# Kernel optimization log

Measured on AMD Instinct MI355X. Metric: run time of the kernel, lower is better.

## Reference

```python
import jax, jax.numpy as jnp
import numpy as np

DIM = 1024
HEADS = 16
DIM_HEAD = 64
INNER = HEADS * DIM_HEAD  # 1024
EPS = 1e-5


def setup_inputs() -> dict:
    key = jax.random.key(0)
    ks = jax.random.split(key, 10)
    b, n1, n2 = 8, 4096, 64
    x = jax.random.normal(ks[0], (b, n1, DIM), dtype=jnp.float32)
    latents = jax.random.normal(ks[1], (b, n2, DIM), dtype=jnp.float32)
    attention_mask = jax.random.randint(ks[2], (b, n1, 1), 0, 2).astype(jnp.float32)
    ln1_g = jnp.ones((DIM,), jnp.float32)
    ln1_b = jnp.zeros((DIM,), jnp.float32)
    ln2_g = jnp.ones((DIM,), jnp.float32)
    ln2_b = jnp.zeros((DIM,), jnp.float32)
    Wq = jax.random.normal(ks[3], (DIM, INNER), dtype=jnp.float32) * 0.02
    Wkv = jax.random.normal(ks[4], (DIM, 2 * INNER), dtype=jnp.float32) * 0.02
    Wout = jax.random.normal(ks[5], (INNER, DIM), dtype=jnp.float32) * 0.02
    return {"x": x, "latents": latents, "attention_mask": attention_mask,
            "ln1_g": ln1_g, "ln1_b": ln1_b, "ln2_g": ln2_g, "ln2_b": ln2_b,
            "Wq": Wq, "Wkv": Wkv, "Wout": Wout}


def _layernorm(t, g, b):
    mu = jnp.mean(t, axis=-1, keepdims=True)
    var = jnp.mean(jnp.square(t - mu), axis=-1, keepdims=True)
    return (t - mu) * jax.lax.rsqrt(var + EPS) * g + b


def _split_heads(t):
    b, n, _ = t.shape
    return t.reshape(b, n, HEADS, DIM_HEAD).transpose(0, 2, 1, 3)  # (b,h,n,d)


def reference(x, latents, attention_mask, ln1_g, ln1_b, ln2_g, ln2_b, Wq, Wkv, Wout):
    xn = _layernorm(x, ln1_g, ln1_b)
    ln = _layernorm(latents, ln2_g, ln2_b)
    b, l, _ = ln.shape

    q = ln @ Wq                                   # (b, n2, inner)
    kv_input = jnp.concatenate([xn, ln], axis=1)  # (b, n1+n2, dim)
    kv = kv_input @ Wkv
    k, v = jnp.split(kv, 2, axis=-1)

    q = _split_heads(q)   # (b,h,n2,d)
    k = _split_heads(k)   # (b,h,n1+n2,d)
    v = _split_heads(v)

    scale = 1.0 / np.sqrt(np.sqrt(DIM_HEAD)).astype(np.float32)
    weight = jnp.einsum('bhqd,bhkd->bhqk', q * scale, k * scale)

    # build additive mask: (b,n1,1) -> (b,1,n1), concat ones for latent keys
    m = jnp.swapaxes(attention_mask, 1, 2)                     # (b,1,n1)
    m = jnp.concatenate([m, jnp.ones_like(m[:, :, :1]).repeat(l, axis=2)], axis=2)
    bias = ((m - 1.0) * 100.0)[:, None]                        # (b,1,1,n1+n2)
    weight = weight + bias

    weight = jax.nn.softmax(weight.astype(jnp.float32), axis=-1).astype(weight.dtype)
    out = jnp.einsum('bhqk,bhkd->bhqd', weight, v)
    out = out.transpose(0, 2, 1, 3).reshape(b, l, INNER)
    return out @ Wout
```

## Files before the change

kernel.cpp:

```cpp
#include <hip/hip_runtime.h>
#include <cstdint>
#include <cstddef>


typedef unsigned short u16;
typedef __bf16 bf16x8 __attribute__((ext_vector_type(8)));
typedef float f32x16 __attribute__((ext_vector_type(16)));

#define MFMA32(a, b, c) __builtin_amdgcn_mfma_f32_32x32x16_bf16((a), (b), (c), 0, 0, 0)

__device__ __forceinline__ u16 f2bf(float f) {
  unsigned u = __builtin_bit_cast(unsigned, f);
  u += 0x7FFFu + ((u >> 16) & 1u);
  return (u16)(u >> 16);
}

__device__ __forceinline__ f32x16 zero16() {
  f32x16 z;
#pragma unroll
  for (int i = 0; i < 16; ++i) z[i] = 0.f;
  return z;
}

#if defined(__has_builtin)
#if __has_builtin(__builtin_amdgcn_global_load_lds)
#define HAVE_GLDS 1
#endif
#endif

__device__ __forceinline__ void async16(const u16* g, u16* lbase, int lane) {
#ifdef HAVE_GLDS
  typedef const __attribute__((address_space(1))) void* gp_t;
  typedef __attribute__((address_space(3))) void* lp_t;
  __builtin_amdgcn_global_load_lds((gp_t)g, (lp_t)lbase, 16, 0, 0);
#else
  *(uint4*)(lbase + lane * 8) = *(const uint4*)g;
#endif
}

__global__ void wtrans(const float* __restrict__ W, u16* __restrict__ Wt, int K, int N) {
  __shared__ float t[32][33];
  int n0 = blockIdx.x * 32, k0 = blockIdx.y * 32;
  int tx = threadIdx.x, ty = threadIdx.y;
#pragma unroll
  for (int i = 0; i < 4; ++i)
    t[ty + 8 * i][tx] = W[(size_t)(k0 + ty + 8 * i) * N + n0 + tx];
  __syncthreads();
#pragma unroll
  for (int i = 0; i < 4; ++i)
    Wt[(size_t)(n0 + ty + 8 * i) * K + k0 + tx] = f2bf(t[tx][ty + 8 * i]);
}

__global__ void ln_kernel(const float* __restrict__ x, const float* __restrict__ lat,
                          const float* __restrict__ g1, const float* __restrict__ b1,
                          const float* __restrict__ g2, const float* __restrict__ b2,
                          u16* __restrict__ kvin, u16* __restrict__ qin) {
  int row = blockIdx.x;
  const float *src, *g, *bb;
  u16 *dst, *dst2 = nullptr;
  if (row < 32768) {
    int b = row >> 12, pos = row & 4095;
    src = x + (size_t)row * 1024;
    dst = kvin + (size_t)(b * 4160 + pos) * 1024;
    g = g1; bb = b1;
  } else {
    int i = row - 32768;
    int b = i >> 6, j = i & 63;
    src = lat + (size_t)i * 1024;
    dst = kvin + (size_t)(b * 4160 + 4096 + j) * 1024;
    dst2 = qin + (size_t)i * 1024;
    g = g2; bb = b2;
  }
  int t = threadIdx.x;
  float4 v = *(const float4*)(src + t * 4);
  float s = v.x + v.y + v.z + v.w;
  float ss = v.x * v.x + v.y * v.y + v.z * v.z + v.w * v.w;
#pragma unroll
  for (int off = 32; off; off >>= 1) {
    s += __shfl_xor(s, off);
    ss += __shfl_xor(ss, off);
  }
  __shared__ float red[8];
  int w = t >> 6;
  if ((t & 63) == 0) { red[w] = s; red[w + 4] = ss; }
  __syncthreads();
  s = red[0] + red[1] + red[2] + red[3];
  ss = red[4] + red[5] + red[6] + red[7];
  float mu = s * (1.f / 1024.f);
  float var = ss * (1.f / 1024.f) - mu * mu;
  float rstd = rsqrtf(var + 1e-5f);
  float4 gv = *(const float4*)(g + t * 4);
  float4 bv = *(const float4*)(bb + t * 4);
  ushort4 o;
  o.x = f2bf((v.x - mu) * rstd * gv.x + bv.x);
  o.y = f2bf((v.y - mu) * rstd * gv.y + bv.y);
  o.z = f2bf((v.z - mu) * rstd * gv.z + bv.z);
  o.w = f2bf((v.w - mu) * rstd * gv.w + bv.w);
  *(ushort4*)(dst + t * 4) = o;
  if (dst2) *(ushort4*)(dst2 + t * 4) = o;
}

template <int EPI>
__global__ void __launch_bounds__(256, 2) gemm128(
    const u16* __restrict__ A, const u16* __restrict__ Bt, int K,
    u16* __restrict__ oK, u16* __restrict__ oV, float* __restrict__ oF) {
  __shared__ __align__(16) u16 lds[18432];
  u16* As = lds;
  u16* Bs = lds + 8192;
  const int tid = threadIdx.x;
  const int lane = tid & 63;
  const int w = tid >> 6;
  const int lc = lane & 31;
  const int hh = lane >> 5;
  const int m0 = blockIdx.y * 128;
  const int n0 = blockIdx.x * 128;
  const int wm = (w >> 1) * 64;
  const int wn = (w & 1) * 64;

  f32x16 acc[2][2];
#pragma unroll
  for (int i = 0; i < 2; ++i)
#pragma unroll
    for (int j = 0; j < 2; ++j) acc[i][j] = zero16();

  const int rsub = lane >> 3;
  const int cslot = lane & 7;

  for (int kt = 0; kt < K; kt += 64) {
    __syncthreads();
#pragma unroll
    for (int i = 0; i < 4; ++i) {
      const int rr = (w * 4 + i) * 8 + rsub;
      const int cA = cslot ^ (rr & 7);
      async16(A + (size_t)(m0 + rr) * K + kt + cA * 8, As + (w * 4 + i) * 512, lane);
      async16(Bt + (size_t)(n0 + rr) * K + kt + cA * 8, Bs + (w * 4 + i) * 512, lane);
    }
    __syncthreads();
    const int am0 = wm + lc, am1 = wm + 32 + lc;
    const int bn0 = wn + lc, bn1 = wn + 32 + lc;
#pragma unroll
    for (int s = 0; s < 4; ++s) {
      const int c = s * 2 + hh;
      bf16x8 a0 = *(const bf16x8*)(As + am0 * 64 + ((c ^ (am0 & 7)) * 8));
      bf16x8 a1 = *(const bf16x8*)(As + am1 * 64 + ((c ^ (am1 & 7)) * 8));
      bf16x8 b0 = *(const bf16x8*)(Bs + bn0 * 64 + ((c ^ (bn0 & 7)) * 8));
      bf16x8 b1 = *(const bf16x8*)(Bs + bn1 * 64 + ((c ^ (bn1 & 7)) * 8));
      acc[0][0] = MFMA32(a0, b0, acc[0][0]);
      acc[0][1] = MFMA32(a0, b1, acc[0][1]);
      acc[1][0] = MFMA32(a1, b0, acc[1][0]);
      acc[1][1] = MFMA32(a1, b1, acc[1][1]);
    }
  }

  if constexpr (EPI == 2) {
#pragma unroll
    for (int mt = 0; mt < 2; ++mt)
#pragma unroll
      for (int nt = 0; nt < 2; ++nt)
#pragma unroll
        for (int r = 0; r < 16; ++r) {
          int grow = m0 + wm + mt * 32 + (r & 3) + 8 * (r >> 2) + 4 * hh;
          int gcol = n0 + wn + nt * 32 + lc;
          oF[(size_t)grow * 1024 + gcol] = acc[mt][nt][r];
        }
  } else {
    const bool kstyle = (EPI == 1) || (blockIdx.x < 8);
    if (kstyle) {
      constexpr int SEQ = (EPI == 1) ? 64 : 4160;
      constexpr float SC = (EPI == 1) ? 0.125f : 1.0f;
#pragma unroll
      for (int mt = 0; mt < 2; ++mt)
#pragma unroll
        for (int nt = 0; nt < 2; ++nt)
#pragma unroll
          for (int r = 0; r < 16; ++r) {
            int grow = m0 + wm + mt * 32 + (r & 3) + 8 * (r >> 2) + 4 * hh;
            int gcol = n0 + wn + nt * 32 + lc;
            int bb = grow / SEQ, rr2 = grow - bb * SEQ;
            int h = gcol >> 6, d = gcol & 63;
            oK[(((size_t)(bb * 16 + h)) * SEQ + rr2) * 64 + d] = f2bf(acc[mt][nt][r] * SC);
          }
    } else {
      __syncthreads();
      u16* T = lds;
#pragma unroll
      for (int mt = 0; mt < 2; ++mt)
#pragma unroll
        for (int nt = 0; nt < 2; ++nt) {
          int nl = wn + nt * 32 + lc;
#pragma unroll
          for (int r4 = 0; r4 < 4; ++r4) {
            int ml = wm + mt * 32 + 8 * r4 + 4 * hh;
            ushort4 pk;
            pk.x = f2bf(acc[mt][nt][4 * r4 + 0]);
            pk.y = f2bf(acc[mt][nt][4 * r4 + 1]);
            pk.z = f2bf(acc[mt][nt][4 * r4 + 2]);
            pk.w = f2bf(acc[mt][nt][4 * r4 + 3]);
            *(ushort4*)(T + nl * 144 + ml) = pk;
          }
        }
      __syncthreads();
#pragma unroll
      for (int rr2 = 0; rr2 < 8; ++rr2) {
        int sig = tid + rr2 * 256;
        int n = sig >> 4, cm = (sig & 15) << 3;
        uint4 v = *(const uint4*)(T + n * 144 + cm);
        int gcol = n0 + n - 1024;
        int h = gcol >> 6, d = gcol & 63;
        int grow = m0 + cm;
        int bb = grow / 4160, key = grow - bb * 4160;
        *(uint4*)(oV + (((size_t)(bb * 16 + h)) * 64 + d) * 4160 + key) = v;
      }
    }
  }
}

__global__ void __launch_bounds__(256) attn_kernel(
    const u16* __restrict__ Q, const u16* __restrict__ Kb,
    const u16* __restrict__ Vt, const float* __restrict__ mask,
    float* __restrict__ nums, float* __restrict__ dens) {
  __shared__ __align__(16) u16 Ps[16384];
  __shared__ float Osum[4160];
  __shared__ float den_s[256];
  const int p = blockIdx.x;
  const int bh = p >> 2, s = p & 3;
  const int b = bh >> 4;
  const int tid = threadIdx.x, lane = tid & 63, w = tid >> 6;
  const int hh = lane >> 5, lc = lane & 31;

  for (int i = tid; i < 4160; i += 256) Osum[i] = 0.f;
  den_s[tid] = 0.f;
  __syncthreads();

  const u16* Qb = Q + (size_t)bh * 4096;
  const u16* Kbb = Kb + (size_t)bh * 266240;
  const u16* Vtb = Vt + (size_t)bh * 266240;

  bf16x8 qf[2][4];
#pragma unroll
  for (int qt = 0; qt < 2; ++qt)
#pragma unroll
    for (int ks = 0; ks < 4; ++ks)
      qf[qt][ks] = *(const bf16x8*)(Qb + (qt * 32 + lc) * 64 + ks * 16 + hh * 8);

  f32x16 o[2][2];
#pragma unroll
  for (int i = 0; i < 2; ++i)
#pragma unroll
    for (int j = 0; j < 2; ++j) o[i][j] = zero16();
  float den0 = 0.f, den1 = 0.f;
  u16* Pw = Ps + w * 4096;
  const int t0 = (s == 0) ? 0 : (16 * s + 1);
  const int t1 = (s == 3) ? 65 : (16 * (s + 1) + 1);

  for (int t = t0 + w; t < t1; t += 4) {
    const int key0 = t * 64;
    const int keyl = key0 + lane;
    float bias_v = 0.f;
    if (keyl < 4096) bias_v = (mask[b * 4096 + keyl] - 1.f) * 100.f;

    bf16x8 kf[2][4];
#pragma unroll
    for (int ktt = 0; ktt < 2; ++ktt)
#pragma unroll
      for (int ks = 0; ks < 4; ++ks)
        kf[ktt][ks] = *(const bf16x8*)(Kbb + (size_t)(key0 + ktt * 32 + lc) * 64 + ks * 16 + hh * 8);

    f32x16 st[2][2];
#pragma unroll
    for (int i = 0; i < 2; ++i)
#pragma unroll
      for (int j = 0; j < 2; ++j) st[i][j] = zero16();
#pragma unroll
    for (int ks = 0; ks < 4; ++ks) {
      st[0][0] = MFMA32(kf[0][ks], qf[0][ks], st[0][0]);
      st[0][1] = MFMA32(kf[0][ks], qf[1][ks], st[0][1]);
      st[1][0] = MFMA32(kf[1][ks], qf[0][ks], st[1][0]);
      st[1][1] = MFMA32(kf[1][ks], qf[1][ks], st[1][1]);
    }

#pragma unroll
    for (int ktt = 0; ktt < 2; ++ktt) {
      float bb[16];
#pragma unroll
      for (int r = 0; r < 16; ++r)
        bb[r] = __shfl(bias_v, ktt * 32 + (r & 3) + 8 * (r >> 2) + 4 * hh);
#pragma unroll
      for (int qt = 0; qt < 2; ++qt) {
        const int q = qt * 32 + lc;
        float dsum = 0.f;
#pragma unroll
        for (int r4 = 0; r4 < 4; ++r4) {
          float e0 = __expf(st[ktt][qt][4 * r4 + 0] + bb[4 * r4 + 0]);
          float e1 = __expf(st[ktt][qt][4 * r4 + 1] + bb[4 * r4 + 1]);
          float e2 = __expf(st[ktt][qt][4 * r4 + 2] + bb[4 * r4 + 2]);
          float e3 = __expf(st[ktt][qt][4 * r4 + 3] + bb[4 * r4 + 3]);
          dsum += e0 + e1 + e2 + e3;
          ushort4 pk;
          pk.x = f2bf(e0); pk.y = f2bf(e1); pk.z = f2bf(e2); pk.w = f2bf(e3);
          const int c = ktt * 4 + r4;
          *(ushort4*)(Pw + q * 64 + ((c ^ (q & 7)) * 8) + 4 * hh) = pk;
        }
        if (qt == 0) den0 += dsum; else den1 += dsum;
      }
    }

#pragma unroll
    for (int ks = 0; ks < 4; ++ks) {
      const int c = ks * 2 + hh;
      bf16x8 p0 = *(const bf16x8*)(Pw + lc * 64 + ((c ^ (lc & 7)) * 8));
      bf16x8 p1 = *(const bf16x8*)(Pw + (32 + lc) * 64 + ((c ^ (lc & 7)) * 8));
      bf16x8 v0 = *(const bf16x8*)(Vtb + (size_t)lc * 4160 + key0 + ks * 16 + hh * 8);
      bf16x8 v1 = *(const bf16x8*)(Vtb + (size_t)(32 + lc) * 4160 + key0 + ks * 16 + hh * 8);
      o[0][0] = MFMA32(p0, v0, o[0][0]);
      o[0][1] = MFMA32(p0, v1, o[0][1]);
      o[1][0] = MFMA32(p1, v0, o[1][0]);
      o[1][1] = MFMA32(p1, v1, o[1][1]);
    }
  }

#pragma unroll
  for (int qt = 0; qt < 2; ++qt)
#pragma unroll
    for (int dt = 0; dt < 2; ++dt)
#pragma unroll
      for (int r = 0; r < 16; ++r) {
        int row = qt * 32 + (r & 3) + 8 * (r >> 2) + 4 * hh;
        int col = dt * 32 + lc;
        atomicAdd(&Osum[row * 65 + col], o[qt][dt][r]);
      }
  den0 += __shfl_xor(den0, 32);
  den1 += __shfl_xor(den1, 32);
  if (lane < 32) {
    den_s[w * 64 + lc] = den0;
    den_s[w * 64 + 32 + lc] = den1;
  }
  __syncthreads();
  float* np_ = nums + (size_t)p * 4096;
  for (int i = tid; i < 4096; i += 256)
    np_[i] = Osum[(i >> 6) * 65 + (i & 63)];
  if (tid < 64)
    dens[p * 64 + tid] = den_s[tid] + den_s[64 + tid] + den_s[128 + tid] + den_s[192 + tid];
}

__global__ void combine_kernel(const float* __restrict__ nums, const float* __restrict__ dens,
                               u16* __restrict__ O) {
  int idx = blockIdx.x * 256 + threadIdx.x;
  int bh = idx >> 12;
  int q = (idx >> 6) & 63, d = idx & 63;
  float n = 0.f, dn = 0.f;
#pragma unroll
  for (int s = 0; s < 4; ++s) {
    n += nums[(size_t)(bh * 4 + s) * 4096 + q * 64 + d];
    dn += dens[(bh * 4 + s) * 64 + q];
  }
  int b = bh >> 4, h = bh & 15;
  O[((size_t)(b * 64 + q) * 16 + h) * 64 + d] = f2bf(n / dn);
}

extern "C" void kernel_launch(void* const* d_in, const int* in_sizes, int n_in,
                              void* d_out, int out_size, void* d_ws, size_t ws_size,
                              hipStream_t stream) {
  (void)in_sizes; (void)n_in; (void)out_size; (void)ws_size;
  const float* x    = (const float*)d_in[0];
  const float* lat  = (const float*)d_in[1];
  const float* mask = (const float*)d_in[2];
  const float* g1   = (const float*)d_in[3];
  const float* b1   = (const float*)d_in[4];
  const float* g2   = (const float*)d_in[5];
  const float* b2   = (const float*)d_in[6];
  const float* Wq   = (const float*)d_in[7];
  const float* Wkv  = (const float*)d_in[8];
  const float* Wout = (const float*)d_in[9];
  float* out = (float*)d_out;

  unsigned char* w = (unsigned char*)d_ws;
  u16* kvin = (u16*)w;   w += (size_t)33280 * 1024 * 2;
  u16* qin = (u16*)w;    w += (size_t)512 * 1024 * 2;
  u16* WqT = (u16*)w;    w += (size_t)1024 * 1024 * 2;
  u16* WkvT = (u16*)w;   w += (size_t)2048 * 1024 * 2;
  u16* WoutT = (u16*)w;  w += (size_t)1024 * 1024 * 2;
  u16* Kbuf = (u16*)w;   w += (size_t)33280 * 1024 * 2;
  u16* Vtb = (u16*)w;    w += (size_t)33280 * 1024 * 2;
  u16* Qbuf = (u16*)w;   w += (size_t)512 * 1024 * 2;
  u16* Obuf = (u16*)w;   w += (size_t)512 * 1024 * 2;
  float* nums = (float*)w; w += (size_t)512 * 4096 * 4;
  float* dens = (float*)w; w += (size_t)512 * 64 * 4;

  wtrans<<<dim3(32, 32), dim3(32, 8), 0, stream>>>(Wq, WqT, 1024, 1024);
  wtrans<<<dim3(64, 32), dim3(32, 8), 0, stream>>>(Wkv, WkvT, 1024, 2048);
  wtrans<<<dim3(32, 32), dim3(32, 8), 0, stream>>>(Wout, WoutT, 1024, 1024);
  ln_kernel<<<33280, 256, 0, stream>>>(x, lat, g1, b1, g2, b2, kvin, qin);
  gemm128<0><<<dim3(16, 260), 256, 0, stream>>>(kvin, WkvT, 1024, Kbuf, Vtb, nullptr);
  gemm128<1><<<dim3(8, 4), 256, 0, stream>>>(qin, WqT, 1024, Qbuf, nullptr, nullptr);
  attn_kernel<<<512, 256, 0, stream>>>(Qbuf, Kbuf, Vtb, mask, nums, dens);
  combine_kernel<<<2048, 256, 0, stream>>>(nums, dens, Obuf);
  gemm128<2><<<dim3(8, 4), 256, 0, stream>>>(Obuf, WoutT, 1024, nullptr, nullptr, out);
}
```

Before: 501.1 us.

## Stage K/V tiles in LDS for attention, split-K small GEMMs, merge weight transposes

The attention kernel now double-buffers 64-key K and V tiles into LDS with async loads, and all four waves share each tile instead of each wave streaming its own keys from global memory. V is written by the KV GEMM in a tiled 64x64 blocked layout to support this. The small Q and output projections become split-K GEMMs with 4 K-slices plus separate reduce kernels, so they launch 128 blocks instead of 32. The three weight transposes are merged into one launch. The cost is extra launches, partial-sum traffic through global memory, and two block barriers per key tile in attention.

```diff
diff --git a/kernel.cpp b/kernel.cpp
--- a/kernel.cpp
+++ b/kernel.cpp
@@ -38,9 +38,18 @@
 #endif
 }
 
-__global__ void wtrans(const float* __restrict__ W, u16* __restrict__ Wt, int K, int N) {
+__global__ void wtrans_all(const float* __restrict__ Wq, const float* __restrict__ Wkv,
+                           const float* __restrict__ Wout, u16* __restrict__ WqT,
+                           u16* __restrict__ WkvT, u16* __restrict__ WoutT) {
   __shared__ float t[32][33];
-  int n0 = blockIdx.x * 32, k0 = blockIdx.y * 32;
+  const int z = blockIdx.z;
+  const float* W;
+  u16* Wt;
+  int N, nbase;
+  if (z == 0) { W = Wq; Wt = WqT; N = 1024; nbase = 0; }
+  else if (z == 3) { W = Wout; Wt = WoutT; N = 1024; nbase = 0; }
+  else { W = Wkv; Wt = WkvT; N = 2048; nbase = (z - 1) * 1024; }
+  int n0 = nbase + blockIdx.x * 32, k0 = blockIdx.y * 32;
   int tx = threadIdx.x, ty = threadIdx.y;
 #pragma unroll
   for (int i = 0; i < 4; ++i)
@@ -48,7 +57,7 @@
   __syncthreads();
 #pragma unroll
   for (int i = 0; i < 4; ++i)
-    Wt[(size_t)(n0 + ty + 8 * i) * K + k0 + tx] = f2bf(t[tx][ty + 8 * i]);
+    Wt[(size_t)(n0 + ty + 8 * i) * 1024 + k0 + tx] = f2bf(t[tx][ty + 8 * i]);
 }
 
 __global__ void ln_kernel(const float* __restrict__ x, const float* __restrict__ lat,
@@ -102,7 +111,7 @@
 
 template <int EPI>
 __global__ void __launch_bounds__(256, 2) gemm128(
-    const u16* __restrict__ A, const u16* __restrict__ Bt, int K,
+    const u16* __restrict__ A, const u16* __restrict__ Bt, int kLen,
     u16* __restrict__ oK, u16* __restrict__ oV, float* __restrict__ oF) {
   __shared__ __align__(16) u16 lds[18432];
   u16* As = lds;
@@ -116,6 +125,7 @@
   const int n0 = blockIdx.x * 128;
   const int wm = (w >> 1) * 64;
   const int wn = (w & 1) * 64;
+  const int k0 = blockIdx.z * kLen;
 
   f32x16 acc[2][2];
 #pragma unroll
@@ -126,14 +136,14 @@
   const int rsub = lane >> 3;
   const int cslot = lane & 7;
 
-  for (int kt = 0; kt < K; kt += 64) {
+  for (int kt = k0; kt < k0 + kLen; kt += 64) {
     __syncthreads();
 #pragma unroll
     for (int i = 0; i < 4; ++i) {
       const int rr = (w * 4 + i) * 8 + rsub;
       const int cA = cslot ^ (rr & 7);
-      async16(A + (size_t)(m0 + rr) * K + kt + cA * 8, As + (w * 4 + i) * 512, lane);
-      async16(Bt + (size_t)(n0 + rr) * K + kt + cA * 8, Bs + (w * 4 + i) * 512, lane);
+      async16(A + (size_t)(m0 + rr) * 1024 + kt + cA * 8, As + (w * 4 + i) * 512, lane);
+      async16(Bt + (size_t)(n0 + rr) * 1024 + kt + cA * 8, Bs + (w * 4 + i) * 512, lane);
     }
     __syncthreads();
     const int am0 = wm + lc, am1 = wm + 32 + lc;
@@ -153,6 +163,7 @@
   }
 
   if constexpr (EPI == 2) {
+    oF += (size_t)blockIdx.z * (512 * 1024);
 #pragma unroll
     for (int mt = 0; mt < 2; ++mt)
 #pragma unroll
@@ -164,10 +175,7 @@
           oF[(size_t)grow * 1024 + gcol] = acc[mt][nt][r];
         }
   } else {
-    const bool kstyle = (EPI == 1) || (blockIdx.x < 8);
-    if (kstyle) {
-      constexpr int SEQ = (EPI == 1) ? 64 : 4160;
-      constexpr float SC = (EPI == 1) ? 0.125f : 1.0f;
+    if (blockIdx.x < 8) {
 #pragma unroll
       for (int mt = 0; mt < 2; ++mt)
 #pragma unroll
@@ -176,9 +184,9 @@
           for (int r = 0; r < 16; ++r) {
             int grow = m0 + wm + mt * 32 + (r & 3) + 8 * (r >> 2) + 4 * hh;
             int gcol = n0 + wn + nt * 32 + lc;
-            int bb = grow / SEQ, rr2 = grow - bb * SEQ;
+            int bb = grow / 4160, rr2 = grow - bb * 4160;
             int h = gcol >> 6, d = gcol & 63;
-            oK[(((size_t)(bb * 16 + h)) * SEQ + rr2) * 64 + d] = f2bf(acc[mt][nt][r] * SC);
+            oK[(((size_t)(bb * 16 + h)) * 4160 + rr2) * 64 + d] = f2bf(acc[mt][nt][r]);
           }
     } else {
       __syncthreads();
@@ -209,138 +217,135 @@
         int h = gcol >> 6, d = gcol & 63;
         int grow = m0 + cm;
         int bb = grow / 4160, key = grow - bb * 4160;
-        *(uint4*)(oV + (((size_t)(bb * 16 + h)) * 64 + d) * 4160 + key) = v;
+        int tt = key >> 6, kk = key & 63;
+        *(uint4*)(oV + ((((size_t)(bb * 16 + h) * 65 + tt) * 64 + d) * 64 + kk)) = v;
       }
     }
   }
+}
+
+__global__ void qreduce(const float* __restrict__ P, u16* __restrict__ Qbuf) {
+  int idx = blockIdx.x * 256 + threadIdx.x;
+  float s = P[idx] + P[idx + 524288] + P[idx + 2 * 524288] + P[idx + 3 * 524288];
+  int row = idx >> 10, col = idx & 1023;
+  int b = row >> 6, q = row & 63, h = col >> 6, d = col & 63;
+  Qbuf[((size_t)(b * 16 + h) * 64 + q) * 64 + d] = f2bf(s * 0.125f);
+}
+
+__global__ void oreduce(const float* __restrict__ P, float* __restrict__ out) {
+  int idx = blockIdx.x * 256 + threadIdx.x;
+  out[idx] = P[idx] + P[idx + 524288] + P[idx + 2 * 524288] + P[idx + 3 * 524288];
 }
 
 __global__ void __launch_bounds__(256) attn_kernel(
     const u16* __restrict__ Q, const u16* __restrict__ Kb,
-    const u16* __restrict__ Vt, const float* __restrict__ mask,
+    const u16* __restrict__ VB, const float* __restrict__ mask,
     float* __restrict__ nums, float* __restrict__ dens) {
-  __shared__ __align__(16) u16 Ps[16384];
-  __shared__ float Osum[4160];
-  __shared__ float den_s[256];
+  __shared__ __align__(16) u16 KT[2][4096];
+  __shared__ __align__(16) u16 VT[2][4096];
+  __shared__ __align__(16) u16 PT[4096];
+  __shared__ float den_s[128];
   const int p = blockIdx.x;
   const int bh = p >> 2, s = p & 3;
   const int b = bh >> 4;
   const int tid = threadIdx.x, lane = tid & 63, w = tid >> 6;
   const int hh = lane >> 5, lc = lane & 31;
-
-  for (int i = tid; i < 4160; i += 256) Osum[i] = 0.f;
-  den_s[tid] = 0.f;
-  __syncthreads();
+  const int rsub = lane >> 3, cslot = lane & 7;
+  const int kh = w >> 1, qh = w & 1;
+  const int qh2 = w >> 1, dh2 = w & 1;
 
   const u16* Qb = Q + (size_t)bh * 4096;
   const u16* Kbb = Kb + (size_t)bh * 266240;
-  const u16* Vtb = Vt + (size_t)bh * 266240;
-
-  bf16x8 qf[2][4];
-#pragma unroll
-  for (int qt = 0; qt < 2; ++qt)
-#pragma unroll
-    for (int ks = 0; ks < 4; ++ks)
-      qf[qt][ks] = *(const bf16x8*)(Qb + (qt * 32 + lc) * 64 + ks * 16 + hh * 8);
-
-  f32x16 o[2][2];
-#pragma unroll
-  for (int i = 0; i < 2; ++i)
-#pragma unroll
-    for (int j = 0; j < 2; ++j) o[i][j] = zero16();
-  float den0 = 0.f, den1 = 0.f;
-  u16* Pw = Ps + w * 4096;
+  const u16* Vbb = VB + (size_t)bh * 266240;
+
+  bf16x8 qf[4];
+#pragma unroll
+  for (int ks = 0; ks < 4; ++ks)
+    qf[ks] = *(const bf16x8*)(Qb + (qh * 32 + lc) * 64 + ks * 16 + hh * 8);
+
+  f32x16 o = zero16();
+  float den_reg = 0.f;
   const int t0 = (s == 0) ? 0 : (16 * s + 1);
-  const int t1 = (s == 3) ? 65 : (16 * (s + 1) + 1);
-
-  for (int t = t0 + w; t < t1; t += 4) {
-    const int key0 = t * 64;
-    const int keyl = key0 + lane;
+  const int t1 = (s == 3) ? 65 : (16 * s + 17);
+
+  auto stage = [&](int t, int buf) {
+    const u16* ksrc = Kbb + (size_t)t * 4096;
+    const u16* vsrc = Vbb + (size_t)t * 4096;
+    const int soff = rsub * 64 + ((cslot ^ rsub) * 8);
+#pragma unroll
+    for (int i = 0; i < 2; ++i) {
+      const int c = w * 2 + i;
+      async16(ksrc + c * 512 + soff, KT[buf] + c * 512, lane);
+      async16(vsrc + c * 512 + soff, VT[buf] + c * 512, lane);
+    }
+  };
+
+  stage(t0, 0);
+  for (int t = t0; t < t1; ++t) {
+    const int buf = (t - t0) & 1;
+    __syncthreads();
+    if (t + 1 < t1) stage(t + 1, buf ^ 1);
+
     float bias_v = 0.f;
-    if (keyl < 4096) bias_v = (mask[b * 4096 + keyl] - 1.f) * 100.f;
-
-    bf16x8 kf[2][4];
-#pragma unroll
-    for (int ktt = 0; ktt < 2; ++ktt)
-#pragma unroll
-      for (int ks = 0; ks < 4; ++ks)
-        kf[ktt][ks] = *(const bf16x8*)(Kbb + (size_t)(key0 + ktt * 32 + lc) * 64 + ks * 16 + hh * 8);
-
-    f32x16 st[2][2];
-#pragma unroll
-    for (int i = 0; i < 2; ++i)
-#pragma unroll
-      for (int j = 0; j < 2; ++j) st[i][j] = zero16();
-#pragma unroll
-    for (int ks = 0; ks < 4; ++ks) {
-      st[0][0] = MFMA32(kf[0][ks], qf[0][ks], st[0][0]);
-      st[0][1] = MFMA32(kf[0][ks], qf[1][ks], st[0][1]);
-      st[1][0] = MFMA32(kf[1][ks], qf[0][ks], st[1][0]);
-      st[1][1] = MFMA32(kf[1][ks], qf[1][ks], st[1][1]);
-    }
-
-#pragma unroll
-    for (int ktt = 0; ktt < 2; ++ktt) {
-      float bb[16];
-#pragma unroll
-      for (int r = 0; r < 16; ++r)
-        bb[r] = __shfl(bias_v, ktt * 32 + (r & 3) + 8 * (r >> 2) + 4 * hh);
-#pragma unroll
-      for (int qt = 0; qt < 2; ++qt) {
-        const int q = qt * 32 + lc;
-        float dsum = 0.f;
-#pragma unroll
-        for (int r4 = 0; r4 < 4; ++r4) {
-          float e0 = __expf(st[ktt][qt][4 * r4 + 0] + bb[4 * r4 + 0]);
-          float e1 = __expf(st[ktt][qt][4 * r4 + 1] + bb[4 * r4 + 1]);
-          float e2 = __expf(st[ktt][qt][4 * r4 + 2] + bb[4 * r4 + 2]);
-          float e3 = __expf(st[ktt][qt][4 * r4 + 3] + bb[4 * r4 + 3]);
-          dsum += e0 + e1 + e2 + e3;
-          ushort4 pk;
-          pk.x = f2bf(e0); pk.y = f2bf(e1); pk.z = f2bf(e2); pk.w = f2bf(e3);
-          const int c = ktt * 4 + r4;
-          *(ushort4*)(Pw + q * 64 + ((c ^ (q & 7)) * 8) + 4 * hh) = pk;
-        }
-        if (qt == 0) den0 += dsum; else den1 += dsum;
-      }
-    }
-
+    {
+      int key_l = t * 64 + kh * 32 + lc;
+      if (key_l < 4096) bias_v = (mask[b * 4096 + key_l] - 1.f) * 100.f;
+    }
+
+    f32x16 st = zero16();
+    const int R = kh * 32 + lc;
 #pragma unroll
     for (int ks = 0; ks < 4; ++ks) {
       const int c = ks * 2 + hh;
-      bf16x8 p0 = *(const bf16x8*)(Pw + lc * 64 + ((c ^ (lc & 7)) * 8));
-      bf16x8 p1 = *(const bf16x8*)(Pw + (32 + lc) * 64 + ((c ^ (lc & 7)) * 8));
-      bf16x8 v0 = *(const bf16x8*)(Vtb + (size_t)lc * 4160 + key0 + ks * 16 + hh * 8);
-      bf16x8 v1 = *(const bf16x8*)(Vtb + (size_t)(32 + lc) * 4160 + key0 + ks * 16 + hh * 8);
-      o[0][0] = MFMA32(p0, v0, o[0][0]);
-      o[0][1] = MFMA32(p0, v1, o[0][1]);
-      o[1][0] = MFMA32(p1, v0, o[1][0]);
-      o[1][1] = MFMA32(p1, v1, o[1][1]);
-    }
-  }
-
-#pragma unroll
-  for (int qt = 0; qt < 2; ++qt)
-#pragma unroll
-    for (int dt = 0; dt < 2; ++dt)
-#pragma unroll
-      for (int r = 0; r < 16; ++r) {
-        int row = qt * 32 + (r & 3) + 8 * (r >> 2) + 4 * hh;
-        int col = dt * 32 + lc;
-        atomicAdd(&Osum[row * 65 + col], o[qt][dt][r]);
-      }
-  den0 += __shfl_xor(den0, 32);
-  den1 += __shfl_xor(den1, 32);
-  if (lane < 32) {
-    den_s[w * 64 + lc] = den0;
-    den_s[w * 64 + 32 + lc] = den1;
-  }
+      bf16x8 kfr = *(const bf16x8*)(KT[buf] + R * 64 + ((c ^ (R & 7)) * 8));
+      st = MFMA32(kfr, qf[ks], st);
+    }
+
+    const int q = qh * 32 + lc;
+    float dsum = 0.f;
+#pragma unroll
+    for (int r4 = 0; r4 < 4; ++r4) {
+      float bb0 = __shfl(bias_v, 0 + 8 * r4 + 4 * hh);
+      float bb1 = __shfl(bias_v, 1 + 8 * r4 + 4 * hh);
+      float bb2 = __shfl(bias_v, 2 + 8 * r4 + 4 * hh);
+      float bb3 = __shfl(bias_v, 3 + 8 * r4 + 4 * hh);
+      float e0 = __expf(st[4 * r4 + 0] + bb0);
+      float e1 = __expf(st[4 * r4 + 1] + bb1);
+      float e2 = __expf(st[4 * r4 + 2] + bb2);
+      float e3 = __expf(st[4 * r4 + 3] + bb3);
+      dsum += e0 + e1 + e2 + e3;
+      ushort4 pk;
+      pk.x = f2bf(e0); pk.y = f2bf(e1); pk.z = f2bf(e2); pk.w = f2bf(e3);
+      const int cblk = kh * 4 + r4;
+      *(ushort4*)(PT + q * 64 + ((cblk ^ (q & 7)) * 8) + 4 * hh) = pk;
+    }
+    den_reg += dsum;
+    __syncthreads();
+
+    const int qr = qh2 * 32 + lc;
+    const int dr = dh2 * 32 + lc;
+#pragma unroll
+    for (int ks = 0; ks < 4; ++ks) {
+      const int c = ks * 2 + hh;
+      bf16x8 pf = *(const bf16x8*)(PT + qr * 64 + ((c ^ (qr & 7)) * 8));
+      bf16x8 vf = *(const bf16x8*)(VT[buf] + dr * 64 + ((c ^ (dr & 7)) * 8));
+      o = MFMA32(pf, vf, o);
+    }
+  }
+
+  float* np_ = nums + (size_t)p * 4096;
+#pragma unroll
+  for (int r = 0; r < 16; ++r) {
+    int row = qh2 * 32 + (r & 3) + 8 * (r >> 2) + 4 * hh;
+    np_[row * 64 + dh2 * 32 + lc] = o[r];
+  }
+  den_reg += __shfl_xor(den_reg, 32);
+  if (lane < 32) den_s[w * 32 + lc] = den_reg;
   __syncthreads();
-  float* np_ = nums + (size_t)p * 4096;
-  for (int i = tid; i < 4096; i += 256)
-    np_[i] = Osum[(i >> 6) * 65 + (i & 63)];
-  if (tid < 64)
-    dens[p * 64 + tid] = den_s[tid] + den_s[64 + tid] + den_s[128 + tid] + den_s[192 + tid];
+  if (tid < 64) {
+    int g = tid >> 5, l = tid & 31;
+    dens[p * 64 + tid] = den_s[g * 32 + l] + den_s[(g + 2) * 32 + l];
+  }
 }
 
 __global__ void combine_kernel(const float* __restrict__ nums, const float* __restrict__ dens,
@@ -381,19 +386,20 @@
   u16* WkvT = (u16*)w;   w += (size_t)2048 * 1024 * 2;
   u16* WoutT = (u16*)w;  w += (size_t)1024 * 1024 * 2;
   u16* Kbuf = (u16*)w;   w += (size_t)33280 * 1024 * 2;
-  u16* Vtb = (u16*)w;    w += (size_t)33280 * 1024 * 2;
+  u16* Vbuf = (u16*)w;   w += (size_t)33280 * 1024 * 2;
   u16* Qbuf = (u16*)w;   w += (size_t)512 * 1024 * 2;
   u16* Obuf = (u16*)w;   w += (size_t)512 * 1024 * 2;
+  float* part = (float*)w; w += (size_t)4 * 512 * 1024 * 4;
   float* nums = (float*)w; w += (size_t)512 * 4096 * 4;
   float* dens = (float*)w; w += (size_t)512 * 64 * 4;
 
-  wtrans<<<dim3(32, 32), dim3(32, 8), 0, stream>>>(Wq, WqT, 1024, 1024);
-  wtrans<<<dim3(64, 32), dim3(32, 8), 0, stream>>>(Wkv, WkvT, 1024, 2048);
-  wtrans<<<dim3(32, 32), dim3(32, 8), 0, stream>>>(Wout, WoutT, 1024, 1024);
+  wtrans_all<<<dim3(32, 32, 4), dim3(32, 8), 0, stream>>>(Wq, Wkv, Wout, WqT, WkvT, WoutT);
   ln_kernel<<<33280, 256, 0, stream>>>(x, lat, g1, b1, g2, b2, kvin, qin);
-  gemm128<0><<<dim3(16, 260), 256, 0, stream>>>(kvin, WkvT, 1024, Kbuf, Vtb, nullptr);
-  gemm128<1><<<dim3(8, 4), 256, 0, stream>>>(qin, WqT, 1024, Qbuf, nullptr, nullptr);
-  attn_kernel<<<512, 256, 0, stream>>>(Qbuf, Kbuf, Vtb, mask, nums, dens);
+  gemm128<0><<<dim3(16, 260, 1), 256, 0, stream>>>(kvin, WkvT, 1024, Kbuf, Vbuf, nullptr);
+  gemm128<2><<<dim3(8, 4, 4), 256, 0, stream>>>(qin, WqT, 256, nullptr, nullptr, part);
+  qreduce<<<2048, 256, 0, stream>>>(part, Qbuf);
+  attn_kernel<<<512, 256, 0, stream>>>(Qbuf, Kbuf, Vbuf, mask, nums, dens);
   combine_kernel<<<2048, 256, 0, stream>>>(nums, dens, Obuf);
-  gemm128<2><<<dim3(8, 4), 256, 0, stream>>>(Obuf, WoutT, 1024, nullptr, nullptr, out);
-}
+  gemm128<2><<<dim3(8, 4, 4), 256, 0, stream>>>(Obuf, WoutT, 256, nullptr, nullptr, part);
+  oreduce<<<2048, 256, 0, stream>>>(part, out);
+}
```

After: 437.5 us. 12.7% less time.
